# Performance work log

Measured on AMD Instinct MI355X. Metric: run time of the kernel, lower is better.

The kernel has to match this reference:

```python
import jax, jax.numpy as jnp
import numpy as np

B, N, C, H = 2, 2048, 1024, 16
D = C // H
SCALE = D ** -0.5


def setup_inputs() -> dict:
    key = jax.random.key(0)
    ks = jax.random.split(key, 5)
    x = jax.random.normal(ks[0], (B, N, C), dtype=jnp.float32)
    # causal mask, broadcast over batch: True = attend
    attention_mask = jnp.broadcast_to(jnp.tril(jnp.ones((N, N), dtype=bool)), (B, N, N))
    w_qkv = jax.random.normal(ks[1], (3 * C, C), dtype=jnp.float32) * (C ** -0.5)
    b_qkv = jax.random.normal(ks[2], (3 * C,), dtype=jnp.float32) * 0.02
    w_proj = jax.random.normal(ks[3], (C, C), dtype=jnp.float32) * (C ** -0.5)
    b_proj = jax.random.normal(ks[4], (C,), dtype=jnp.float32) * 0.02
    return {"x": x, "attention_mask": attention_mask, "w_qkv": w_qkv,
            "b_qkv": b_qkv, "w_proj": w_proj, "b_proj": b_proj}


def reference(x, attention_mask, w_qkv, b_qkv, w_proj, b_proj):
    b, n, c = x.shape
    qkv = x @ w_qkv.T + b_qkv                      # [B,N,3C]
    qkv = qkv.reshape(b, n, 3, H, D).transpose(2, 0, 3, 1, 4)  # [3,B,H,N,D]
    q, k, v = qkv[0], qkv[1], qkv[2]
    dots = jnp.einsum('bhid,bhjd->bhij', q, k) * SCALE
    mask_value = -jnp.finfo(dots.dtype).max
    dots = jnp.where(attention_mask[:, None, :, :], dots, mask_value)
    attn = jax.nn.softmax(dots.astype(jnp.float32), axis=-1).astype(dots.dtype)
    out = jnp.einsum('bhij,bhjd->bhid', attn, v)   # [B,H,N,D]
    # NOTE: original code reshapes WITHOUT transposing heads back - faithful.
    out = out.reshape(b, n, c)
    return out @ w_proj.T + b_proj
```

## Files before the change

kernel.cpp:

```cpp
#include <hip/hip_runtime.h>
#include <hip/hip_bf16.h>
#include <stdint.h>

#define SL_F 0.18033688011112043f

typedef unsigned short u16;
typedef unsigned int u32;
typedef __attribute__((ext_vector_type(8))) short bf16x8;
typedef __attribute__((ext_vector_type(4))) float f32x4;

__device__ __forceinline__ u16 f2bf(float f) {
    union { float f; u32 u; } v; v.f = f;
    return (u16)((v.u + 0x7fffu + ((v.u >> 16) & 1u)) >> 16);
}
__device__ __forceinline__ u32 pack2bf(float a, float b) {
    union { __hip_bfloat162 h; u32 u; } p;
    p.h = __float22bfloat162_rn(make_float2(a, b));
    return p.u;
}

__device__ __forceinline__ void gl_lds16(const u16* g, u16* l) {
    __builtin_amdgcn_global_load_lds(
        (const __attribute__((address_space(1))) u32*)g,
        (__attribute__((address_space(3))) u32*)l, 16, 0, 0);
}

__global__ __launch_bounds__(256) void convert_k(
    const float* __restrict__ x, const float* __restrict__ w1,
    const float* __restrict__ w2,
    u16* __restrict__ xb, u16* __restrict__ w1b, u16* __restrict__ w2b)
{
    const int t = blockIdx.x * 256 + threadIdx.x;
    const int XA = 524288, XW1 = 393216;
    const float* src; u16* dst; int s;
    if (t < XA)            { src = x;  dst = xb;  s = t; }
    else if (t < XA + XW1) { src = w1; dst = w1b; s = t - XA; }
    else                   { src = w2; dst = w2b; s = t - XA - XW1; }
    const int c = s >> 6;
    const int u = s & 63;
    const int l = (u >> 2) + 16 * (u & 3);
    const int g = c >> 5, kb = c & 31;
    const int row = g * 16 + (l & 15);
    const int k0 = kb * 32 + (l >> 4) * 8;
    const float4 v0 = *(const float4*)&src[(size_t)row * 1024 + k0];
    const float4 v1 = *(const float4*)&src[(size_t)row * 1024 + k0 + 4];
    uint4 o;
    o.x = pack2bf(v0.x, v0.y); o.y = pack2bf(v0.z, v0.w);
    o.z = pack2bf(v1.x, v1.y); o.w = pack2bf(v1.z, v1.w);
    *(uint4*)&dst[((size_t)c * 64 + l) * 8] = o;
}

__global__ __launch_bounds__(256) void qkv_gemm(
    const u16* __restrict__ A, const u16* __restrict__ Bw,
    const float* __restrict__ bias,
    u16* __restrict__ Qb, u16* __restrict__ Kb, u16* __restrict__ VTb)
{
    __shared__ __align__(16) u16 Al[2][8 * 512];
    __shared__ __align__(16) u16 Bl[2][8 * 512];
    const int tid = threadIdx.x;
    const int lane = tid & 63;
    const int w = tid >> 6;
    const int la = lane & 15, qd = lane >> 4;
    const int m0 = blockIdx.y * 128;
    const int n0 = blockIdx.x * 128;
    const int wm = (w >> 1) * 64, wn = (w & 1) * 64;

    const u16* Ag0 = A + ((size_t)((m0 >> 4) + 2 * w) * 32) * 512 + lane * 8;
    const u16* Ag1 = Ag0 + 32 * 512;
    const u16* Bg0 = Bw + ((size_t)((n0 >> 4) + 2 * w) * 32) * 512 + lane * 8;
    const u16* Bg1 = Bg0 + 32 * 512;

    auto stage = [&](int k0, int b) {
        const size_t ko = (size_t)(k0 >> 5) * 512;
        gl_lds16(Ag0 + ko, &Al[b][(2 * w) * 512]);
        gl_lds16(Ag1 + ko, &Al[b][(2 * w + 1) * 512]);
        gl_lds16(Bg0 + ko, &Bl[b][(2 * w) * 512]);
        gl_lds16(Bg1 + ko, &Bl[b][(2 * w + 1) * 512]);
    };

    f32x4 acc[4][4] = {};
    int buf = 0;
    stage(0, 0);

    for (int k0 = 0; k0 < 1024; k0 += 32) {
        __syncthreads();
        if (k0 + 32 < 1024) stage(k0 + 32, buf ^ 1);

        bf16x8 af[4], bfr[4];
#pragma unroll
        for (int i = 0; i < 4; i++)
            af[i] = *(const bf16x8*)&Al[buf][(((unsigned)wm >> 4) + i) * 512 + lane * 8];
#pragma unroll
        for (int j = 0; j < 4; j++)
            bfr[j] = *(const bf16x8*)&Bl[buf][(((unsigned)wn >> 4) + j) * 512 + lane * 8];
#pragma unroll
        for (int i = 0; i < 4; i++)
#pragma unroll
            for (int j = 0; j < 4; j++)
                acc[i][j] = __builtin_amdgcn_mfma_f32_16x16x32_bf16(
                    af[i], bfr[j], acc[i][j], 0, 0, 0);
        buf ^= 1;
    }

    const int b_ = m0 >> 11;
    const int nb = (m0 & 2047) + wm;
#pragma unroll
    for (int j = 0; j < 4; j++) {
        const int colb = n0 + wn + j * 16;
        const int col = colb + la;
        const float bv = bias[col];
        const int t = colb >> 10;
        const int hd = col & 1023, h = hd >> 6, d = hd & 63;
        const int bh = b_ * 16 + h;
        if (t == 0) {
            u16* QB = Qb + ((size_t)bh * 2048 + nb) * 64 + d;
#pragma unroll
            for (int i = 0; i < 4; i++)
#pragma unroll
                for (int r = 0; r < 4; r++)
                    QB[(i * 16 + qd * 4 + r) * 64] =
                        f2bf((acc[i][j][r] + bv) * SL_F);
        } else if (t == 1) {
            u16* KB = Kb + (size_t)bh * 131072
                    + (size_t)((nb >> 4) * 2 + (d >> 5)) * 512 + (d & 31);
#pragma unroll
            for (int i = 0; i < 4; i++)
#pragma unroll
                for (int r = 0; r < 4; r++)
                    KB[i * 1024 + (qd * 4 + r) * 32] = f2bf(acc[i][j][r] + bv);
        } else {
            u16* VB = VTb + (size_t)bh * 131072
                    + (size_t)(d >> 4) * 32768 + (d & 15) * 32;
#pragma unroll
            for (int i = 0; i < 4; i++)
#pragma unroll
                for (int r = 0; r < 4; r++)
                    VB[((nb >> 5) + (i >> 1)) * 512 + (i & 1) * 16 + qd * 4 + r]
                        = f2bf(acc[i][j][r] + bv);
        }
    }
}

__global__ __launch_bounds__(256) void proj_gemm(
    const u16* __restrict__ A, const u16* __restrict__ Bw,
    const float* __restrict__ bias, float* __restrict__ Out)
{
    __shared__ __align__(16) u16 Al[2][16 * 512];
    __shared__ __align__(16) u16 Bl[2][8 * 512];
    const int tid = threadIdx.x;
    const int lane = tid & 63;
    const int w = tid >> 6;
    const int la = lane & 15, qd = lane >> 4;
    const int K = 1024;
    const int m0 = blockIdx.y * 128;
    const int n0 = blockIdx.x * 64;
    const int wm = (w >> 1) * 64, wn = (w & 1) * 32;

    const u16* Ab[4];
#pragma unroll
    for (int t = 0; t < 4; t++) {
        const int ck = 4 * w + t, g = ck >> 1, h = ck & 1;
        Ab[t] = A + (((size_t)(m0 >> 4) + g) * 32 + h) * 512 + lane * 8;
    }
    const u16* Bg = Bw + ((size_t)((n0 >> 4) + w) * 32) * 512 + lane * 8;

    auto stage = [&](int k0, int b) {
#pragma unroll
        for (int t = 0; t < 4; t++)
            gl_lds16(Ab[t] + (size_t)(k0 >> 5) * 512, &Al[b][(4 * w + t) * 512]);
#pragma unroll
        for (int t = 0; t < 2; t++)
            gl_lds16(Bg + (size_t)((k0 >> 5) + t) * 512, &Bl[b][(2 * w + t) * 512]);
    };

    f32x4 acc[4][2] = {};
    int buf = 0;
    stage(0, 0);

    for (int k0 = 0; k0 < K; k0 += 64) {
        __syncthreads();
        if (k0 + 64 < K) stage(k0 + 64, buf ^ 1);

        bf16x8 af[4][2], bfr[2][2];
#pragma unroll
        for (int i = 0; i < 4; i++) {
            const int g = ((unsigned)wm >> 4) + i;
#pragma unroll
            for (int h = 0; h < 2; h++)
                af[i][h] = *(const bf16x8*)&Al[buf][(g * 2 + h) * 512 + lane * 8];
        }
#pragma unroll
        for (int j = 0; j < 2; j++) {
            const int g = ((unsigned)wn >> 4) + j;
#pragma unroll
            for (int h = 0; h < 2; h++)
                bfr[j][h] = *(const bf16x8*)&Bl[buf][(g * 2 + h) * 512 + lane * 8];
        }
#pragma unroll
        for (int i = 0; i < 4; i++)
#pragma unroll
            for (int j = 0; j < 2; j++) {
                f32x4 c = acc[i][j];
                c = __builtin_amdgcn_mfma_f32_16x16x32_bf16(af[i][0], bfr[j][0], c, 0, 0, 0);
                c = __builtin_amdgcn_mfma_f32_16x16x32_bf16(af[i][1], bfr[j][1], c, 0, 0, 0);
                acc[i][j] = c;
            }
        buf ^= 1;
    }

#pragma unroll
    for (int j = 0; j < 2; j++) {
        const int col = n0 + wn + j * 16 + la;
        const float bv = bias[col];
#pragma unroll
        for (int i = 0; i < 4; i++)
#pragma unroll
            for (int r = 0; r < 4; r++) {
                const int row = m0 + wm + i * 16 + qd * 4 + r;
                Out[(size_t)row * 1024 + col] = acc[i][j][r] + bv;
            }
    }
}

__global__ __launch_bounds__(256, 1) void attn_k(
    const u16* __restrict__ Qb, const u16* __restrict__ Kb,
    const u16* __restrict__ VTb, u16* __restrict__ Ob)
{
    __shared__ __align__(16) u16 Kl[2][16 * 512];
    __shared__ __align__(16) u16 Vl[2][16 * 512];
    __shared__ __align__(16) u16 Pl[4][2][16 * 72];
    const int bh = blockIdx.x & 31;
    const int pairT = blockIdx.x >> 5;
    const int tid = threadIdx.x;
    const int lane = tid & 63;
    const int w = tid >> 6;
    const int la = lane & 15, qd = lane >> 4;

    const int perm = (lane & 15) * 32 + (lane >> 4) * 8;
    const u16* Kbh = Kb + (size_t)bh * 131072 + perm;
    const u16* Vbh = VTb + (size_t)bh * 131072 + perm;
    u16* PwA = &Pl[w][0][0];
    u16* PwB = &Pl[w][1][0];

    auto stage = [&](int j0, int b) {
#pragma unroll
        for (int t = 0; t < 4; t++) {
            const int ck = 4 * w + t;
            gl_lds16(Kbh + (size_t)((j0 >> 3) + ck) * 512, &Kl[b][ck * 512]);
            gl_lds16(Vbh + (size_t)((ck >> 2) * 64 + (j0 >> 5) + (ck & 3)) * 512,
                     &Vl[b][ck * 512]);
        }
    };

    int buf = 0;
    stage(0, 0);

    for (int half = 0; half < 2; half++) {
        const int tile = (half == 0) ? pairT : 15 - pairT;
        const int q0 = tile * 128 + w * 32;
        const int jmax = tile * 128;
        const int qrowA = q0 + la;
        const int qrowB = q0 + 16 + la;

        const u16* Qp = Qb + ((size_t)bh * 2048 + q0 + la) * 64 + qd * 8;
        const bf16x8 qfA0 = *(const bf16x8*)Qp;
        const bf16x8 qfA1 = *(const bf16x8*)(Qp + 32);
        const bf16x8 qfB0 = *(const bf16x8*)(Qp + 16 * 64);
        const bf16x8 qfB1 = *(const bf16x8*)(Qp + 16 * 64 + 32);

        f32x4 oA[4] = {}, oB[4] = {};
        float lsumA = 0.f, lsumB = 0.f;

        for (int j0 = 0; j0 <= jmax; j0 += 128) {
            __syncthreads();

            const int nj = (j0 + 128 <= jmax) ? (j0 + 128) : ((half == 0) ? 0 : -1);
            if (nj >= 0) stage(nj, buf ^ 1);

            f32x4 sA[8], sB[8];
#pragma unroll
            for (int c = 0; c < 8; c++) {
                const bf16x8 kf0 = *(const bf16x8*)&Kl[buf][(c * 2 + 0) * 512 + lane * 8];
                const bf16x8 kf1 = *(const bf16x8*)&Kl[buf][(c * 2 + 1) * 512 + lane * 8];
                f32x4 zA = {}, zB = {};
                zA = __builtin_amdgcn_mfma_f32_16x16x32_bf16(kf0, qfA0, zA, 0, 0, 0);
                zA = __builtin_amdgcn_mfma_f32_16x16x32_bf16(kf1, qfA1, zA, 0, 0, 0);
                zB = __builtin_amdgcn_mfma_f32_16x16x32_bf16(kf0, qfB0, zB, 0, 0, 0);
                zB = __builtin_amdgcn_mfma_f32_16x16x32_bf16(kf1, qfB1, zB, 0, 0, 0);
                sA[c] = zA; sB[c] = zB;
            }

            if (j0 == jmax) {
#pragma unroll
                for (int c = 0; c < 8; c++)
#pragma unroll
                    for (int r = 0; r < 4; r++) {
                        const int j = j0 + c * 16 + qd * 4 + r;
                        float vA = sA[c][r], vB = sB[c][r];
                        vA = (j > qrowA) ? -1e30f : vA;
                        vB = (j > qrowB) ? -1e30f : vB;
                        sA[c][r] = __builtin_amdgcn_exp2f(vA);
                        sB[c][r] = __builtin_amdgcn_exp2f(vB);
                    }
            } else {
#pragma unroll
                for (int c = 0; c < 8; c++)
#pragma unroll
                    for (int r = 0; r < 4; r++) {
                        sA[c][r] = __builtin_amdgcn_exp2f(sA[c][r]);
                        sB[c][r] = __builtin_amdgcn_exp2f(sB[c][r]);
                    }
            }
#pragma unroll
            for (int c = 0; c < 8; c++)
#pragma unroll
                for (int r = 0; r < 4; r++) {
                    lsumA += sA[c][r];
                    lsumB += sB[c][r];
                }

#pragma unroll
            for (int hh = 0; hh < 2; hh++) {
#pragma unroll
                for (int c = 0; c < 4; c++) {
                    uint2 pwA, pwB;
                    pwA.x = pack2bf(sA[hh * 4 + c][0], sA[hh * 4 + c][1]);
                    pwA.y = pack2bf(sA[hh * 4 + c][2], sA[hh * 4 + c][3]);
                    pwB.x = pack2bf(sB[hh * 4 + c][0], sB[hh * 4 + c][1]);
                    pwB.y = pack2bf(sB[hh * 4 + c][2], sB[hh * 4 + c][3]);
                    *(uint2*)&PwA[la * 72 + c * 16 + qd * 4] = pwA;
                    *(uint2*)&PwB[la * 72 + c * 16 + qd * 4] = pwB;
                }
                const bf16x8 pfA0 = *(const bf16x8*)&PwA[la * 72 + qd * 8];
                const bf16x8 pfA1 = *(const bf16x8*)&PwA[la * 72 + 32 + qd * 8];
                const bf16x8 pfB0 = *(const bf16x8*)&PwB[la * 72 + qd * 8];
                const bf16x8 pfB1 = *(const bf16x8*)&PwB[la * 72 + 32 + qd * 8];
#pragma unroll
                for (int c2 = 0; c2 < 4; c2++) {
                    const bf16x8 vf0 = *(const bf16x8*)&Vl[buf][(c2 * 4 + hh * 2 + 0) * 512 + lane * 8];
                    const bf16x8 vf1 = *(const bf16x8*)&Vl[buf][(c2 * 4 + hh * 2 + 1) * 512 + lane * 8];
                    oA[c2] = __builtin_amdgcn_mfma_f32_16x16x32_bf16(pfA0, vf0, oA[c2], 0, 0, 0);
                    oA[c2] = __builtin_amdgcn_mfma_f32_16x16x32_bf16(pfA1, vf1, oA[c2], 0, 0, 0);
                    oB[c2] = __builtin_amdgcn_mfma_f32_16x16x32_bf16(pfB0, vf0, oB[c2], 0, 0, 0);
                    oB[c2] = __builtin_amdgcn_mfma_f32_16x16x32_bf16(pfB1, vf1, oB[c2], 0, 0, 0);
                }
            }
            buf ^= 1;
        }

        lsumA += __shfl_xor(lsumA, 16, 64);
        lsumA += __shfl_xor(lsumA, 32, 64);
        lsumB += __shfl_xor(lsumB, 16, 64);
        lsumB += __shfl_xor(lsumB, 32, 64);
        float rinvA[4], rinvB[4];
#pragma unroll
        for (int r = 0; r < 4; r++) {
            rinvA[r] = 1.0f / __shfl(lsumA, qd * 4 + r, 64);
            rinvB[r] = 1.0f / __shfl(lsumB, qd * 4 + r, 64);
        }

        const int m = bh * 128 + (q0 >> 4);
        const int mm = m & 15;
        u16* Ot = Ob + ((size_t)(m >> 4) * 32) * 512;
#pragma unroll
        for (int c2 = 0; c2 < 4; c2++)
#pragma unroll
            for (int r = 0; r < 4; r++) {
                const int kk5 = (qd * 4 + r) * 2 + (c2 >> 1);
                const int s3 = (c2 * 2 + (la >> 3)) & 3;
                const size_t base = (size_t)kk5 * 512 + 16 * s3 * 8 + (la & 7);
                Ot[base + mm * 8]       = f2bf(oA[c2][r] * rinvA[r]);
                Ot[base + (mm + 1) * 8] = f2bf(oB[c2][r] * rinvB[r]);
            }
    }
}

extern "C" void kernel_launch(void* const* d_in, const int* in_sizes, int n_in,
                              void* d_out, int out_size, void* d_ws, size_t ws_size,
                              hipStream_t stream)
{
    const float* x     = (const float*)d_in[0];
    const float* wqkv  = (const float*)d_in[2];
    const float* bqkv  = (const float*)d_in[3];
    const float* wproj = (const float*)d_in[4];
    const float* bproj = (const float*)d_in[5];
    float* out = (float*)d_out;

    u16* ws     = (u16*)d_ws;
    u16* xb     = ws;
    u16* wqkvb  = xb + 4096 * 1024;
    u16* wprojb = wqkvb + 3072 * 1024;
    u16* Qb     = wprojb + 1024 * 1024;
    u16* Kb     = Qb + 32 * 2048 * 64;
    u16* VTb    = Kb + 32 * 2048 * 64;
    u16* Ob     = VTb + 32 * 2048 * 64;

    convert_k<<<dim3(4096), dim3(256), 0, stream>>>(
        x, wqkv, wproj, xb, wqkvb, wprojb);

    qkv_gemm<<<dim3(24, 32), dim3(256), 0, stream>>>(
        xb, wqkvb, bqkv, Qb, Kb, VTb);

    attn_k<<<dim3(256), dim3(256), 0, stream>>>(Qb, Kb, VTb, Ob);

    proj_gemm<<<dim3(16, 32), dim3(256), 0, stream>>>(
        Ob, wprojb, bproj, out);
}
```

Before: 195.2 us.

## Split attention into one query tile per block with 64-key steps and per-wave causal skip

Each block now handles a single 128-row query tile instead of a paired light/heavy tile, and the grid doubles to 512 blocks with launch bounds raised to two blocks per CU. Key/value staging shrinks to 64-key chunks, halving the LDS footprint. Each wave skips chunks lying entirely above its causal diagonal, and MFMA sections are wrapped in raised scheduling priority. The aim is more occupancy and parallelism plus less wasted masked work, at the cost of losing the explicit load balancing from tile pairing and doing more barriers per key.

New measurement: 196.4 us. About the same (+0.6%).

```diff
diff --git a/kernel.cpp b/kernel.cpp
--- a/kernel.cpp
+++ b/kernel.cpp
@@ -222,15 +222,16 @@
     }
 }
 
-__global__ __launch_bounds__(256, 1) void attn_k(
+__global__ __launch_bounds__(256, 2) void attn_k(
     const u16* __restrict__ Qb, const u16* __restrict__ Kb,
     const u16* __restrict__ VTb, u16* __restrict__ Ob)
 {
-    __shared__ __align__(16) u16 Kl[2][16 * 512];
-    __shared__ __align__(16) u16 Vl[2][16 * 512];
+    __shared__ __align__(16) u16 Kl[2][8 * 512];
+    __shared__ __align__(16) u16 Vl[2][8 * 512];
     __shared__ __align__(16) u16 Pl[4][2][16 * 72];
     const int bh = blockIdx.x & 31;
-    const int pairT = blockIdx.x >> 5;
+    const int s = (blockIdx.x >> 5) & 15;
+    const int T = (s < 8) ? s : 23 - s;
     const int tid = threadIdx.x;
     const int lane = tid & 63;
     const int w = tid >> 6;
@@ -242,44 +243,46 @@
     u16* PwA = &Pl[w][0][0];
     u16* PwB = &Pl[w][1][0];
 
-    auto stage = [&](int j0, int b) {
+    auto stage = [&](int jt, int b) {
 #pragma unroll
         for (int t = 0; t < 4; t++) {
             const int ck = 4 * w + t;
-            gl_lds16(Kbh + (size_t)((j0 >> 3) + ck) * 512, &Kl[b][ck * 512]);
-            gl_lds16(Vbh + (size_t)((ck >> 2) * 64 + (j0 >> 5) + (ck & 3)) * 512,
-                     &Vl[b][ck * 512]);
+            if (ck < 8) {
+                gl_lds16(Kbh + (size_t)(jt * 8 + ck) * 512, &Kl[b][ck * 512]);
+            } else {
+                const int cv = ck - 8;
+                gl_lds16(Vbh + (size_t)((cv >> 1) * 64 + jt * 2 + (cv & 1)) * 512,
+                         &Vl[b][cv * 512]);
+            }
         }
     };
+
+    const int q0 = T * 128 + w * 32;
+    const int qrowA = q0 + la;
+    const int qrowB = q0 + 16 + la;
+    const int JT = 2 * T + 2;
+
+    const u16* Qp = Qb + ((size_t)bh * 2048 + q0 + la) * 64 + qd * 8;
+    const bf16x8 qfA0 = *(const bf16x8*)Qp;
+    const bf16x8 qfA1 = *(const bf16x8*)(Qp + 32);
+    const bf16x8 qfB0 = *(const bf16x8*)(Qp + 16 * 64);
+    const bf16x8 qfB1 = *(const bf16x8*)(Qp + 16 * 64 + 32);
+
+    f32x4 oA[4] = {}, oB[4] = {};
+    float lsumA = 0.f, lsumB = 0.f;
 
     int buf = 0;
     stage(0, 0);
 
-    for (int half = 0; half < 2; half++) {
-        const int tile = (half == 0) ? pairT : 15 - pairT;
-        const int q0 = tile * 128 + w * 32;
-        const int jmax = tile * 128;
-        const int qrowA = q0 + la;
-        const int qrowB = q0 + 16 + la;
-
-        const u16* Qp = Qb + ((size_t)bh * 2048 + q0 + la) * 64 + qd * 8;
-        const bf16x8 qfA0 = *(const bf16x8*)Qp;
-        const bf16x8 qfA1 = *(const bf16x8*)(Qp + 32);
-        const bf16x8 qfB0 = *(const bf16x8*)(Qp + 16 * 64);
-        const bf16x8 qfB1 = *(const bf16x8*)(Qp + 16 * 64 + 32);
-
-        f32x4 oA[4] = {}, oB[4] = {};
-        float lsumA = 0.f, lsumB = 0.f;
-
-        for (int j0 = 0; j0 <= jmax; j0 += 128) {
-            __syncthreads();
-
-            const int nj = (j0 + 128 <= jmax) ? (j0 + 128) : ((half == 0) ? 0 : -1);
-            if (nj >= 0) stage(nj, buf ^ 1);
-
-            f32x4 sA[8], sB[8];
-#pragma unroll
-            for (int c = 0; c < 8; c++) {
+    for (int jt = 0; jt < JT; ++jt) {
+        __syncthreads();
+        if (jt + 1 < JT) stage(jt + 1, buf ^ 1);
+
+        if (jt * 64 <= q0 + 31) {
+            f32x4 sA[4], sB[4];
+            __builtin_amdgcn_s_setprio(1);
+#pragma unroll
+            for (int c = 0; c < 4; c++) {
                 const bf16x8 kf0 = *(const bf16x8*)&Kl[buf][(c * 2 + 0) * 512 + lane * 8];
                 const bf16x8 kf1 = *(const bf16x8*)&Kl[buf][(c * 2 + 1) * 512 + lane * 8];
                 f32x4 zA = {}, zB = {};
@@ -289,13 +292,14 @@
                 zB = __builtin_amdgcn_mfma_f32_16x16x32_bf16(kf1, qfB1, zB, 0, 0, 0);
                 sA[c] = zA; sB[c] = zB;
             }
-
-            if (j0 == jmax) {
-#pragma unroll
-                for (int c = 0; c < 8; c++)
+            __builtin_amdgcn_s_setprio(0);
+
+            if (jt * 64 + 63 > q0) {
+#pragma unroll
+                for (int c = 0; c < 4; c++)
 #pragma unroll
                     for (int r = 0; r < 4; r++) {
-                        const int j = j0 + c * 16 + qd * 4 + r;
+                        const int j = jt * 64 + c * 16 + qd * 4 + r;
                         float vA = sA[c][r], vB = sB[c][r];
                         vA = (j > qrowA) ? -1e30f : vA;
                         vB = (j > qrowB) ? -1e30f : vB;
@@ -304,7 +308,7 @@
                     }
             } else {
 #pragma unroll
-                for (int c = 0; c < 8; c++)
+                for (int c = 0; c < 4; c++)
 #pragma unroll
                     for (int r = 0; r < 4; r++) {
                         sA[c][r] = __builtin_amdgcn_exp2f(sA[c][r]);
@@ -312,7 +316,7 @@
                     }
             }
 #pragma unroll
-            for (int c = 0; c < 8; c++)
+            for (int c = 0; c < 4; c++)
 #pragma unroll
                 for (int r = 0; r < 4; r++) {
                     lsumA += sA[c][r];
@@ -320,59 +324,56 @@
                 }
 
 #pragma unroll
+            for (int c = 0; c < 4; c++) {
+                uint2 pwA, pwB;
+                pwA.x = pack2bf(sA[c][0], sA[c][1]);
+                pwA.y = pack2bf(sA[c][2], sA[c][3]);
+                pwB.x = pack2bf(sB[c][0], sB[c][1]);
+                pwB.y = pack2bf(sB[c][2], sB[c][3]);
+                *(uint2*)&PwA[la * 72 + c * 16 + qd * 4] = pwA;
+                *(uint2*)&PwB[la * 72 + c * 16 + qd * 4] = pwB;
+            }
+#pragma unroll
             for (int hh = 0; hh < 2; hh++) {
-#pragma unroll
-                for (int c = 0; c < 4; c++) {
-                    uint2 pwA, pwB;
-                    pwA.x = pack2bf(sA[hh * 4 + c][0], sA[hh * 4 + c][1]);
-                    pwA.y = pack2bf(sA[hh * 4 + c][2], sA[hh * 4 + c][3]);
-                    pwB.x = pack2bf(sB[hh * 4 + c][0], sB[hh * 4 + c][1]);
-                    pwB.y = pack2bf(sB[hh * 4 + c][2], sB[hh * 4 + c][3]);
-                    *(uint2*)&PwA[la * 72 + c * 16 + qd * 4] = pwA;
-                    *(uint2*)&PwB[la * 72 + c * 16 + qd * 4] = pwB;
+                const bf16x8 pfA = *(const bf16x8*)&PwA[la * 72 + hh * 32 + qd * 8];
+                const bf16x8 pfB = *(const bf16x8*)&PwB[la * 72 + hh * 32 + qd * 8];
+                __builtin_amdgcn_s_setprio(1);
+#pragma unroll
+                for (int c2 = 0; c2 < 4; c2++) {
+                    const bf16x8 vf = *(const bf16x8*)&Vl[buf][(c2 * 2 + hh) * 512 + lane * 8];
+                    oA[c2] = __builtin_amdgcn_mfma_f32_16x16x32_bf16(pfA, vf, oA[c2], 0, 0, 0);
+                    oB[c2] = __builtin_amdgcn_mfma_f32_16x16x32_bf16(pfB, vf, oB[c2], 0, 0, 0);
                 }
-                const bf16x8 pfA0 = *(const bf16x8*)&PwA[la * 72 + qd * 8];
-                const bf16x8 pfA1 = *(const bf16x8*)&PwA[la * 72 + 32 + qd * 8];
-                const bf16x8 pfB0 = *(const bf16x8*)&PwB[la * 72 + qd * 8];
-                const bf16x8 pfB1 = *(const bf16x8*)&PwB[la * 72 + 32 + qd * 8];
-#pragma unroll
-                for (int c2 = 0; c2 < 4; c2++) {
-                    const bf16x8 vf0 = *(const bf16x8*)&Vl[buf][(c2 * 4 + hh * 2 + 0) * 512 + lane * 8];
-                    const bf16x8 vf1 = *(const bf16x8*)&Vl[buf][(c2 * 4 + hh * 2 + 1) * 512 + lane * 8];
-                    oA[c2] = __builtin_amdgcn_mfma_f32_16x16x32_bf16(pfA0, vf0, oA[c2], 0, 0, 0);
-                    oA[c2] = __builtin_amdgcn_mfma_f32_16x16x32_bf16(pfA1, vf1, oA[c2], 0, 0, 0);
-                    oB[c2] = __builtin_amdgcn_mfma_f32_16x16x32_bf16(pfB0, vf0, oB[c2], 0, 0, 0);
-                    oB[c2] = __builtin_amdgcn_mfma_f32_16x16x32_bf16(pfB1, vf1, oB[c2], 0, 0, 0);
-                }
-            }
-            buf ^= 1;
-        }
-
-        lsumA += __shfl_xor(lsumA, 16, 64);
-        lsumA += __shfl_xor(lsumA, 32, 64);
-        lsumB += __shfl_xor(lsumB, 16, 64);
-        lsumB += __shfl_xor(lsumB, 32, 64);
-        float rinvA[4], rinvB[4];
+                __builtin_amdgcn_s_setprio(0);
+            }
+        }
+        buf ^= 1;
+    }
+
+    lsumA += __shfl_xor(lsumA, 16, 64);
+    lsumA += __shfl_xor(lsumA, 32, 64);
+    lsumB += __shfl_xor(lsumB, 16, 64);
+    lsumB += __shfl_xor(lsumB, 32, 64);
+    float rinvA[4], rinvB[4];
+#pragma unroll
+    for (int r = 0; r < 4; r++) {
+        rinvA[r] = 1.0f / __shfl(lsumA, qd * 4 + r, 64);
+        rinvB[r] = 1.0f / __shfl(lsumB, qd * 4 + r, 64);
+    }
+
+    const int m = bh * 128 + (q0 >> 4);
+    const int mm = m & 15;
+    u16* Ot = Ob + ((size_t)(m >> 4) * 32) * 512;
+#pragma unroll
+    for (int c2 = 0; c2 < 4; c2++)
 #pragma unroll
         for (int r = 0; r < 4; r++) {
-            rinvA[r] = 1.0f / __shfl(lsumA, qd * 4 + r, 64);
-            rinvB[r] = 1.0f / __shfl(lsumB, qd * 4 + r, 64);
-        }
-
-        const int m = bh * 128 + (q0 >> 4);
-        const int mm = m & 15;
-        u16* Ot = Ob + ((size_t)(m >> 4) * 32) * 512;
-#pragma unroll
-        for (int c2 = 0; c2 < 4; c2++)
-#pragma unroll
-            for (int r = 0; r < 4; r++) {
-                const int kk5 = (qd * 4 + r) * 2 + (c2 >> 1);
-                const int s3 = (c2 * 2 + (la >> 3)) & 3;
-                const size_t base = (size_t)kk5 * 512 + 16 * s3 * 8 + (la & 7);
-                Ot[base + mm * 8]       = f2bf(oA[c2][r] * rinvA[r]);
-                Ot[base + (mm + 1) * 8] = f2bf(oB[c2][r] * rinvB[r]);
-            }
-    }
+            const int kk5 = (qd * 4 + r) * 2 + (c2 >> 1);
+            const int s3 = (c2 * 2 + (la >> 3)) & 3;
+            const size_t base = (size_t)kk5 * 512 + 16 * s3 * 8 + (la & 7);
+            Ot[base + mm * 8]       = f2bf(oA[c2][r] * rinvA[r]);
+            Ot[base + (mm + 1) * 8] = f2bf(oB[c2][r] * rinvB[r]);
+        }
 }
 
 extern "C" void kernel_launch(void* const* d_in, const int* in_sizes, int n_in,
@@ -401,7 +402,7 @@
     qkv_gemm<<<dim3(24, 32), dim3(256), 0, stream>>>(
         xb, wqkvb, bqkv, Qb, Kb, VTb);
 
-    attn_k<<<dim3(256), dim3(256), 0, stream>>>(Qb, Kb, VTb, Ob);
+    attn_k<<<dim3(512), dim3(256), 0, stream>>>(Qb, Kb, VTb, Ob);
 
     proj_gemm<<<dim3(16, 32), dim3(256), 0, stream>>>(
         Ob, wprojb, bproj, out);
```
